# Kernel optimization log

Hardware: AMD Instinct MI355X
Metric: run time of the kernel (lower is better)

Reference implementation:

```python
import jax, jax.numpy as jnp
import numpy as np

B, R, S, T, D, DK = 256, 196, 200, 50, 512, 100


def setup_inputs() -> dict:
    key = jax.random.key(0)
    ks = jax.random.split(key, 20)
    inp = {
        'ifeature': jax.random.normal(ks[0], (B, R, D), jnp.float32),
        'tfeature_h': jax.random.normal(ks[1], (B, S, D), jnp.float32),
        'gfeature': jax.random.normal(ks[2], (B, S, D), jnp.float32),
        'efeature': jax.random.normal(ks[3], (B, T, D), jnp.float32),
    }
    # learned params (keras 'random_normal' init ~ stddev 0.05, 'zeros' for biases)
    lens = [R, S, S, T]
    for i in range(4):
        inp[f'w_vi{i}'] = 0.05 * jax.random.normal(ks[4 + 4 * i], (D, DK), jnp.float32)
        inp[f'w_vt{i}'] = 0.05 * jax.random.normal(ks[5 + 4 * i], (D, DK), jnp.float32)
        inp[f'w_p{i}'] = 0.05 * jax.random.normal(ks[6 + 4 * i], (2 * DK, 1), jnp.float32)
        inp[f'b{i}'] = jnp.zeros((lens[i],), jnp.float32)
    return inp


def _attend(feats, w_feat, vec, w_vec, w_p, b, vec_first):
    # feats: [B,N,D], vec: [B,D]. Score = concat(tanh parts) @ w_p + b.
    # concat+dense == split w_p into the two halves and add the partial scores.
    k = w_feat.shape[1]
    sf = jnp.tanh(jnp.einsum('bnd,dk->bnk', feats, w_feat))  # [B,N,k]
    sv = jnp.tanh(vec @ w_vec)                               # [B,k]
    if vec_first:
        wv, wf = w_p[:k, 0], w_p[k:, 0]
    else:
        wf, wv = w_p[:k, 0], w_p[k:, 0]
    score = sf @ wf + (sv @ wv)[:, None] + b                 # [B,N]
    p = jax.nn.softmax(score, axis=-1)
    return jnp.einsum('bn,bnd->bd', p, feats)                # [B,D]


def reference(ifeature, tfeature_h, gfeature, efeature,
              w_vi0, w_vt0, w_p0, b0,
              w_vi1, w_vt1, w_p1, b1,
              w_vi2, w_vt2, w_p2, b2,
              w_vi3, w_vt3, w_p3, b3):
    tfeature = jnp.mean(tfeature_h, axis=1)                  # [B,D]
    # block 0: attend over image regions, concat order (image, text)
    Vi = _attend(ifeature, w_vi0, tfeature, w_vt0, w_p0, b0, vec_first=False)
    # block 1: attend over text tokens, concat order (Vi, text)
    Vt = _attend(tfeature_h, w_vt1, Vi, w_vi1, w_p1, b1, vec_first=True)
    # block 2: attend over group feature with query Vi+Vt
    Vg = _attend(gfeature, w_vt2, Vi + Vt, w_vi2, w_p2, b2, vec_first=True)
    # block 3: attend over title feature with query Vi+Vt
    Ve = _attend(efeature, w_vt3, Vi + Vt, w_vi3, w_p3, b3, vec_first=True)
    return Vi + Vt + 0.5 * Vg + 0.5 * Ve
```

## Files before the change

### kernel.cpp

```cpp
#include <hip/hip_runtime.h>

#define DD 512
#define DKk 100
#define NT 7
#define CHUNK 16
#define MAXN 208
#define LDS_STRIDE 520

typedef __attribute__((ext_vector_type(8))) short short8;
typedef __attribute__((ext_vector_type(4))) short short4v;
typedef __attribute__((ext_vector_type(4))) float f32x4;

struct AttendArgs {
  const float* feats[4];
  const float* wfeat[4];
  const float* wf[4];
  const float* bias[4];
  int   N[4];
  float coef[4];
};

__device__ __forceinline__ short f2bf(float x) {
  unsigned u = __builtin_bit_cast(unsigned, x);
  unsigned r = (u + 0x7fffu + ((u >> 16) & 1u)) >> 16;
  return (short)r;
}

__device__ __forceinline__ float bf2f(unsigned short s) {
  unsigned u = ((unsigned)s) << 16;
  return __builtin_bit_cast(float, u);
}

__device__ __forceinline__ float fast_tanh(float x) {
  const float e = __expf(2.0f * x);
  return 1.0f - 2.0f / (e + 1.0f);
}

__global__ void wprep_kernel(AttendArgs args, unsigned short* __restrict__ wfrag) {
  const int a   = blockIdx.x >> 2;
  const int qtr = blockIdx.x & 3;
  const int tid = threadIdx.x;
  const int lane = tid & 63;
  const int m = lane & 15;
  const int q = lane >> 4;
  const int sub = tid >> 6;
  const int ks  = qtr * 4 + sub;
  __shared__ float wbuf[128 * DKk];
  const float* __restrict__ w = args.wfeat[a] + (size_t)qtr * 128 * DKk;
  #pragma unroll
  for (int i = 0; i < 50; ++i)
    wbuf[i * 256 + tid] = w[i * 256 + tid];
  __syncthreads();
  #pragma unroll
  for (int t = 0; t < NT; ++t) {
    const int col = t * 16 + m;
    short8 v;
    #pragma unroll
    for (int j = 0; j < 8; ++j) {
      const int drel = sub * 32 + q * 8 + j;
      v[j] = (col < DKk) ? f2bf(wbuf[drel * DKk + col]) : (short)0;
    }
    unsigned short* dst = wfrag + (size_t)(((a * NT + t) * 16 + ks) * 512) + lane * 8;
    *reinterpret_cast<short8*>(dst) = v;
  }
}

__global__ __launch_bounds__(512, 2)
void fused_kernel(AttendArgs args, const unsigned short* __restrict__ wfrag,
                  float* __restrict__ out) {
  const int a = blockIdx.x & 3;
  const int b = blockIdx.x >> 2;
  const int tid = threadIdx.x;
  const int lane = tid & 63;
  const int wave = tid >> 6;
  const int m = lane & 15;
  const int q = lane >> 4;
  const int N = args.N[a];
  const float* __restrict__ feats = args.feats[a] + (size_t)b * (size_t)N * DD;
  const float* __restrict__ wfp = args.wf[a];
  const float* __restrict__ bias = args.bias[a];

  __shared__ __align__(16) unsigned short f_lds[2][CHUNK][LDS_STRIDE];
  __shared__ float sc_part[8][MAXN];
  __shared__ __align__(16) float partial[8][DD];
  __shared__ float red[512];

  short8 bfrag[16];
  float wfv = 0.f;
  if (wave < NT) {
    const int col = wave * 16 + m;
    wfv = (col < DKk) ? wfp[col] : 0.f;
    const unsigned short* src = wfrag + (size_t)((a * NT + wave) * 16) * 512 + lane * 8;
    #pragma unroll
    for (int ks = 0; ks < 16; ++ks)
      bfrag[ks] = *reinterpret_cast<const short8*>(src + (size_t)ks * 512);
  } else {
    #pragma unroll
    for (int ks = 0; ks < 16; ++ks) bfrag[ks] = short8(0);
  }

  if (tid < MAXN) sc_part[7][tid] = (tid < N) ? bias[tid] : 0.f;
  {
    const f32x4 z = {0.f, 0.f, 0.f, 0.f};
    *reinterpret_cast<f32x4*>(&partial[wave][lane * 8])     = z;
    *reinterpret_cast<f32x4*>(&partial[wave][lane * 8 + 4]) = z;
  }

  const int nchunks = (N + CHUNK - 1) / CHUNK;

  auto accum = [&](int pb, int n0) {
    float* pp = &partial[wave][lane * 8];
    f32x4 lo = *reinterpret_cast<f32x4*>(pp);
    f32x4 hi = *reinterpret_cast<f32x4*>(pp + 4);
    {
      const int n1 = n0 + wave;
      const float s1 = sc_part[0][n1] + sc_part[1][n1] + sc_part[2][n1] + sc_part[3][n1]
                     + sc_part[4][n1] + sc_part[5][n1] + sc_part[6][n1] + sc_part[7][n1];
      const float e1 = __expf(s1);
      const short8 f1 = *reinterpret_cast<const short8*>(&f_lds[pb][wave][lane * 8]);
      #pragma unroll
      for (int j = 0; j < 4; ++j) {
        lo[j] = fmaf(e1, bf2f((unsigned short)f1[j]),     lo[j]);
        hi[j] = fmaf(e1, bf2f((unsigned short)f1[j + 4]), hi[j]);
      }
    }
    {
      const int n2 = n0 + wave + 8;
      const float s2 = sc_part[0][n2] + sc_part[1][n2] + sc_part[2][n2] + sc_part[3][n2]
                     + sc_part[4][n2] + sc_part[5][n2] + sc_part[6][n2] + sc_part[7][n2];
      const float e2 = __expf(s2);
      const short8 f2 = *reinterpret_cast<const short8*>(&f_lds[pb][wave + 8][lane * 8]);
      #pragma unroll
      for (int j = 0; j < 4; ++j) {
        lo[j] = fmaf(e2, bf2f((unsigned short)f2[j]),     lo[j]);
        hi[j] = fmaf(e2, bf2f((unsigned short)f2[j + 4]), hi[j]);
      }
    }
    *reinterpret_cast<f32x4*>(pp)     = lo;
    *reinterpret_cast<f32x4*>(pp + 4) = hi;
  };

  float4 pf[4];
  #pragma unroll
  for (int it = 0; it < 4; ++it) {
    const int idx = tid + it * 512;
    const int row = idx >> 7;
    const int c4 = idx & 127;
    pf[it] = (row < N)
      ? *reinterpret_cast<const float4*>(feats + (size_t)row * DD + (c4 << 2))
      : make_float4(0.f, 0.f, 0.f, 0.f);
  }

  for (int c = 0; c < nchunks; ++c) {
    const int bufc = c & 1;
    #pragma unroll
    for (int it = 0; it < 4; ++it) {
      const int idx = tid + it * 512;
      const int row = idx >> 7;
      const int c4 = idx & 127;
      short4v pk = { f2bf(pf[it].x), f2bf(pf[it].y), f2bf(pf[it].z), f2bf(pf[it].w) };
      *reinterpret_cast<short4v*>(&f_lds[bufc][row][c4 << 2]) = pk;
    }
    if (c + 1 < nchunks) {
      const int n0n = (c + 1) * CHUNK;
      #pragma unroll
      for (int it = 0; it < 4; ++it) {
        const int idx = tid + it * 512;
        const int row = n0n + (idx >> 7);
        const int c4 = idx & 127;
        pf[it] = (row < N)
          ? *reinterpret_cast<const float4*>(feats + (size_t)row * DD + (c4 << 2))
          : make_float4(0.f, 0.f, 0.f, 0.f);
      }
    }
    __syncthreads();

    if (wave < NT) {
      f32x4 acc = {0.f, 0.f, 0.f, 0.f};
      #pragma unroll
      for (int ks = 0; ks < 16; ++ks) {
        const short8 af = *reinterpret_cast<const short8*>(&f_lds[bufc][m][ks * 32 + q * 8]);
        acc = __builtin_amdgcn_mfma_f32_16x16x32_bf16(af, bfrag[ks], acc, 0, 0, 0);
      }
      float part[4];
      #pragma unroll
      for (int r = 0; r < 4; ++r) part[r] = fast_tanh(acc[r]) * wfv;
      #pragma unroll
      for (int mask = 1; mask <= 8; mask <<= 1) {
        #pragma unroll
        for (int r = 0; r < 4; ++r) part[r] += __shfl_xor(part[r], mask, 64);
      }
      if (m == 0) {
        #pragma unroll
        for (int r = 0; r < 4; ++r) sc_part[wave][c * 16 + q * 4 + r] = part[r];
      }
    }
    if (c > 0) accum(bufc ^ 1, (c - 1) * CHUNK);
    __syncthreads();
  }

  accum((nchunks - 1) & 1, (nchunks - 1) * CHUNK);
  __syncthreads();

  float e = 0.f;
  if (tid < N) {
    const float sval = sc_part[0][tid] + sc_part[1][tid] + sc_part[2][tid] + sc_part[3][tid]
                     + sc_part[4][tid] + sc_part[5][tid] + sc_part[6][tid] + sc_part[7][tid];
    e = __expf(sval);
  }
  red[tid] = e;
  __syncthreads();
  for (int s = 256; s > 0; s >>= 1) {
    if (tid < s) red[tid] += red[tid + s];
    __syncthreads();
  }
  const float scale = args.coef[a] / red[0];

  const float val = partial[0][tid] + partial[1][tid] + partial[2][tid] + partial[3][tid]
                  + partial[4][tid] + partial[5][tid] + partial[6][tid] + partial[7][tid];
  atomicAdd(&out[(size_t)b * DD + tid], val * scale);
}

extern "C" void kernel_launch(void* const* d_in, const int* in_sizes, int n_in,
                              void* d_out, int out_size, void* d_ws, size_t ws_size,
                              hipStream_t stream) {
  AttendArgs args;
  args.feats[0] = (const float*)d_in[0];
  args.wfeat[0] = (const float*)d_in[4];
  args.wf[0]    = (const float*)d_in[6];
  args.bias[0]  = (const float*)d_in[7];
  args.N[0] = 196; args.coef[0] = 1.0f;

  args.feats[1] = (const float*)d_in[1];
  args.wfeat[1] = (const float*)d_in[9];
  args.wf[1]    = (const float*)d_in[10] + 100;
  args.bias[1]  = (const float*)d_in[11];
  args.N[1] = 200; args.coef[1] = 1.0f;

  args.feats[2] = (const float*)d_in[2];
  args.wfeat[2] = (const float*)d_in[13];
  args.wf[2]    = (const float*)d_in[14] + 100;
  args.bias[2]  = (const float*)d_in[15];
  args.N[2] = 200; args.coef[2] = 0.5f;

  args.feats[3] = (const float*)d_in[3];
  args.wfeat[3] = (const float*)d_in[17];
  args.wf[3]    = (const float*)d_in[18] + 100;
  args.bias[3]  = (const float*)d_in[19];
  args.N[3] = 50;  args.coef[3] = 0.5f;

  unsigned short* wfrag = (unsigned short*)d_ws;

  hipMemsetAsync(d_out, 0, (size_t)out_size * sizeof(float), stream);
  wprep_kernel<<<dim3(16), dim3(256), 0, stream>>>(args, wfrag);
  fused_kernel<<<dim3(4 * 256), dim3(512), 0, stream>>>(args, wfrag, (float*)d_out);
}
```

Baseline: 366.7 us.

## Fold weight prep into fused kernel, DPP score reduction, leaner LDS softmax

Drops the separate weight-prep kernel: each block now loads and converts its MFMA weight fragments straight from global memory with strided scalar loads. It also swaps the shuffle-based score reduction for DPP adds, moves the softmax denominator into per-wave running sums instead of a tree reduction, lays partial scores out per row for vectorized reads, and changes the feature load mapping so each lane writes 8 contiguous bf16 values. Launch bounds are raised to 4 blocks per CU. These changes cut a kernel launch, synchronizations and LDS traffic, at the cost of redundant, uncoalesced weight reads in every block and possible register pressure from the higher occupancy target.

```diff
diff --git a/kernel.cpp b/kernel.cpp
--- a/kernel.cpp
+++ b/kernel.cpp
@@ -8,7 +8,6 @@
 #define LDS_STRIDE 520
 
 typedef __attribute__((ext_vector_type(8))) short short8;
-typedef __attribute__((ext_vector_type(4))) short short4v;
 typedef __attribute__((ext_vector_type(4))) float f32x4;
 
 struct AttendArgs {
@@ -25,49 +24,21 @@
   unsigned r = (u + 0x7fffu + ((u >> 16) & 1u)) >> 16;
   return (short)r;
 }
-
 __device__ __forceinline__ float bf2f(unsigned short s) {
   unsigned u = ((unsigned)s) << 16;
   return __builtin_bit_cast(float, u);
 }
-
 __device__ __forceinline__ float fast_tanh(float x) {
   const float e = __expf(2.0f * x);
   return 1.0f - 2.0f / (e + 1.0f);
 }
 
-__global__ void wprep_kernel(AttendArgs args, unsigned short* __restrict__ wfrag) {
-  const int a   = blockIdx.x >> 2;
-  const int qtr = blockIdx.x & 3;
-  const int tid = threadIdx.x;
-  const int lane = tid & 63;
-  const int m = lane & 15;
-  const int q = lane >> 4;
-  const int sub = tid >> 6;
-  const int ks  = qtr * 4 + sub;
-  __shared__ float wbuf[128 * DKk];
-  const float* __restrict__ w = args.wfeat[a] + (size_t)qtr * 128 * DKk;
-  #pragma unroll
-  for (int i = 0; i < 50; ++i)
-    wbuf[i * 256 + tid] = w[i * 256 + tid];
-  __syncthreads();
-  #pragma unroll
-  for (int t = 0; t < NT; ++t) {
-    const int col = t * 16 + m;
-    short8 v;
-    #pragma unroll
-    for (int j = 0; j < 8; ++j) {
-      const int drel = sub * 32 + q * 8 + j;
-      v[j] = (col < DKk) ? f2bf(wbuf[drel * DKk + col]) : (short)0;
-    }
-    unsigned short* dst = wfrag + (size_t)(((a * NT + t) * 16 + ks) * 512) + lane * 8;
-    *reinterpret_cast<short8*>(dst) = v;
-  }
-}
-
-__global__ __launch_bounds__(512, 2)
-void fused_kernel(AttendArgs args, const unsigned short* __restrict__ wfrag,
-                  float* __restrict__ out) {
+#define DPP_ADD(x, CTRL)                                                      \
+  (x) += __builtin_bit_cast(float, __builtin_amdgcn_update_dpp(               \
+             0, __builtin_bit_cast(int, (x)), (CTRL), 0xF, 0xF, true))
+
+__global__ __launch_bounds__(512, 4)
+void fused_kernel(AttendArgs args, float* __restrict__ out) {
   const int a = blockIdx.x & 3;
   const int b = blockIdx.x >> 2;
   const int tid = threadIdx.x;
@@ -77,100 +48,94 @@
   const int q = lane >> 4;
   const int N = args.N[a];
   const float* __restrict__ feats = args.feats[a] + (size_t)b * (size_t)N * DD;
-  const float* __restrict__ wfp = args.wf[a];
-  const float* __restrict__ bias = args.bias[a];
 
   __shared__ __align__(16) unsigned short f_lds[2][CHUNK][LDS_STRIDE];
-  __shared__ float sc_part[8][MAXN];
-  __shared__ __align__(16) float partial[8][DD];
-  __shared__ float red[512];
+  __shared__ __align__(16) float sc2[MAXN][8];
+  __shared__ __align__(16) float pA[8][256];
+  __shared__ __align__(16) float pB[8][256];
+  __shared__ float den8[8];
 
   short8 bfrag[16];
   float wfv = 0.f;
-  if (wave < NT) {
+  {
     const int col = wave * 16 + m;
-    wfv = (col < DKk) ? wfp[col] : 0.f;
-    const unsigned short* src = wfrag + (size_t)((a * NT + wave) * 16) * 512 + lane * 8;
+    const bool ok = (wave < NT) && (col < DKk);
+    if (ok) wfv = args.wf[a][col];
+    const float* __restrict__ wp = args.wfeat[a] + col;
     #pragma unroll
-    for (int ks = 0; ks < 16; ++ks)
-      bfrag[ks] = *reinterpret_cast<const short8*>(src + (size_t)ks * 512);
-  } else {
-    #pragma unroll
-    for (int ks = 0; ks < 16; ++ks) bfrag[ks] = short8(0);
-  }
-
-  if (tid < MAXN) sc_part[7][tid] = (tid < N) ? bias[tid] : 0.f;
+    for (int ks = 0; ks < 16; ++ks) {
+      short8 v;
+      #pragma unroll
+      for (int j = 0; j < 8; ++j)
+        v[j] = ok ? f2bf(wp[(size_t)(ks * 32 + q * 8 + j) * DKk]) : (short)0;
+      bfrag[ks] = v;
+    }
+  }
+
+  if (tid < MAXN) sc2[tid][7] = (tid < N) ? args.bias[a][tid] : -1e30f;
   {
     const f32x4 z = {0.f, 0.f, 0.f, 0.f};
-    *reinterpret_cast<f32x4*>(&partial[wave][lane * 8])     = z;
-    *reinterpret_cast<f32x4*>(&partial[wave][lane * 8 + 4]) = z;
+    *reinterpret_cast<f32x4*>(&pA[wave][lane * 4]) = z;
+    *reinterpret_cast<f32x4*>(&pB[wave][lane * 4]) = z;
   }
 
   const int nchunks = (N + CHUNK - 1) / CHUNK;
+  float den = 0.f;
 
   auto accum = [&](int pb, int n0) {
-    float* pp = &partial[wave][lane * 8];
-    f32x4 lo = *reinterpret_cast<f32x4*>(pp);
-    f32x4 hi = *reinterpret_cast<f32x4*>(pp + 4);
-    {
-      const int n1 = n0 + wave;
-      const float s1 = sc_part[0][n1] + sc_part[1][n1] + sc_part[2][n1] + sc_part[3][n1]
-                     + sc_part[4][n1] + sc_part[5][n1] + sc_part[6][n1] + sc_part[7][n1];
-      const float e1 = __expf(s1);
-      const short8 f1 = *reinterpret_cast<const short8*>(&f_lds[pb][wave][lane * 8]);
-      #pragma unroll
-      for (int j = 0; j < 4; ++j) {
-        lo[j] = fmaf(e1, bf2f((unsigned short)f1[j]),     lo[j]);
-        hi[j] = fmaf(e1, bf2f((unsigned short)f1[j + 4]), hi[j]);
-      }
-    }
-    {
-      const int n2 = n0 + wave + 8;
-      const float s2 = sc_part[0][n2] + sc_part[1][n2] + sc_part[2][n2] + sc_part[3][n2]
-                     + sc_part[4][n2] + sc_part[5][n2] + sc_part[6][n2] + sc_part[7][n2];
-      const float e2 = __expf(s2);
-      const short8 f2 = *reinterpret_cast<const short8*>(&f_lds[pb][wave + 8][lane * 8]);
-      #pragma unroll
-      for (int j = 0; j < 4; ++j) {
-        lo[j] = fmaf(e2, bf2f((unsigned short)f2[j]),     lo[j]);
-        hi[j] = fmaf(e2, bf2f((unsigned short)f2[j + 4]), hi[j]);
-      }
-    }
-    *reinterpret_cast<f32x4*>(pp)     = lo;
-    *reinterpret_cast<f32x4*>(pp + 4) = hi;
+    const int n1 = n0 + wave, n2 = n0 + wave + 8;
+    const f32x4 sa1 = *reinterpret_cast<const f32x4*>(&sc2[n1][0]);
+    const f32x4 sb1 = *reinterpret_cast<const f32x4*>(&sc2[n1][4]);
+    const f32x4 sa2 = *reinterpret_cast<const f32x4*>(&sc2[n2][0]);
+    const f32x4 sb2 = *reinterpret_cast<const f32x4*>(&sc2[n2][4]);
+    const float e1 = __expf(sa1[0] + sa1[1] + sa1[2] + sa1[3] +
+                            sb1[0] + sb1[1] + sb1[2] + sb1[3]);
+    const float e2 = __expf(sa2[0] + sa2[1] + sa2[2] + sa2[3] +
+                            sb2[0] + sb2[1] + sb2[2] + sb2[3]);
+    den += e1 + e2;
+    const short8 f1 = *reinterpret_cast<const short8*>(&f_lds[pb][wave][lane * 8]);
+    const short8 f2 = *reinterpret_cast<const short8*>(&f_lds[pb][wave + 8][lane * 8]);
+    f32x4 lo = *reinterpret_cast<const f32x4*>(&pA[wave][lane * 4]);
+    f32x4 hi = *reinterpret_cast<const f32x4*>(&pB[wave][lane * 4]);
+    #pragma unroll
+    for (int j = 0; j < 4; ++j) {
+      lo[j] = fmaf(e1, bf2f((unsigned short)f1[j]),
+              fmaf(e2, bf2f((unsigned short)f2[j]), lo[j]));
+      hi[j] = fmaf(e1, bf2f((unsigned short)f1[j + 4]),
+              fmaf(e2, bf2f((unsigned short)f2[j + 4]), hi[j]));
+    }
+    *reinterpret_cast<f32x4*>(&pA[wave][lane * 4]) = lo;
+    *reinterpret_cast<f32x4*>(&pB[wave][lane * 4]) = hi;
   };
 
   float4 pf[4];
   #pragma unroll
-  for (int it = 0; it < 4; ++it) {
-    const int idx = tid + it * 512;
-    const int row = idx >> 7;
-    const int c4 = idx & 127;
-    pf[it] = (row < N)
-      ? *reinterpret_cast<const float4*>(feats + (size_t)row * DD + (c4 << 2))
-      : make_float4(0.f, 0.f, 0.f, 0.f);
+  for (int h = 0; h < 2; ++h) {
+    const int row = wave + h * 8;
+    const float* src = feats + (size_t)row * DD + lane * 8;
+    const bool ok = row < N;
+    pf[2 * h]     = ok ? *reinterpret_cast<const float4*>(src)     : make_float4(0.f, 0.f, 0.f, 0.f);
+    pf[2 * h + 1] = ok ? *reinterpret_cast<const float4*>(src + 4) : make_float4(0.f, 0.f, 0.f, 0.f);
   }
 
   for (int c = 0; c < nchunks; ++c) {
     const int bufc = c & 1;
     #pragma unroll
-    for (int it = 0; it < 4; ++it) {
-      const int idx = tid + it * 512;
-      const int row = idx >> 7;
-      const int c4 = idx & 127;
-      short4v pk = { f2bf(pf[it].x), f2bf(pf[it].y), f2bf(pf[it].z), f2bf(pf[it].w) };
-      *reinterpret_cast<short4v*>(&f_lds[bufc][row][c4 << 2]) = pk;
+    for (int h = 0; h < 2; ++h) {
+      const float4 va = pf[2 * h], vb = pf[2 * h + 1];
+      short8 pk = { f2bf(va.x), f2bf(va.y), f2bf(va.z), f2bf(va.w),
+                    f2bf(vb.x), f2bf(vb.y), f2bf(vb.z), f2bf(vb.w) };
+      *reinterpret_cast<short8*>(&f_lds[bufc][wave + h * 8][lane * 8]) = pk;
     }
     if (c + 1 < nchunks) {
       const int n0n = (c + 1) * CHUNK;
       #pragma unroll
-      for (int it = 0; it < 4; ++it) {
-        const int idx = tid + it * 512;
-        const int row = n0n + (idx >> 7);
-        const int c4 = idx & 127;
-        pf[it] = (row < N)
-          ? *reinterpret_cast<const float4*>(feats + (size_t)row * DD + (c4 << 2))
-          : make_float4(0.f, 0.f, 0.f, 0.f);
+      for (int h = 0; h < 2; ++h) {
+        const int row = n0n + wave + h * 8;
+        const float* src = feats + (size_t)row * DD + lane * 8;
+        const bool ok = row < N;
+        pf[2 * h]     = ok ? *reinterpret_cast<const float4*>(src)     : make_float4(0.f, 0.f, 0.f, 0.f);
+        pf[2 * h + 1] = ok ? *reinterpret_cast<const float4*>(src + 4) : make_float4(0.f, 0.f, 0.f, 0.f);
       }
     }
     __syncthreads();
@@ -182,42 +147,37 @@
         const short8 af = *reinterpret_cast<const short8*>(&f_lds[bufc][m][ks * 32 + q * 8]);
         acc = __builtin_amdgcn_mfma_f32_16x16x32_bf16(af, bfrag[ks], acc, 0, 0, 0);
       }
-      float part[4];
-      #pragma unroll
-      for (int r = 0; r < 4; ++r) part[r] = fast_tanh(acc[r]) * wfv;
-      #pragma unroll
-      for (int mask = 1; mask <= 8; mask <<= 1) {
-        #pragma unroll
-        for (int r = 0; r < 4; ++r) part[r] += __shfl_xor(part[r], mask, 64);
-      }
-      if (m == 0) {
-        #pragma unroll
-        for (int r = 0; r < 4; ++r) sc_part[wave][c * 16 + q * 4 + r] = part[r];
-      }
+      float p0 = fast_tanh(acc[0]) * wfv;
+      float p1 = fast_tanh(acc[1]) * wfv;
+      float p2 = fast_tanh(acc[2]) * wfv;
+      float p3 = fast_tanh(acc[3]) * wfv;
+      DPP_ADD(p0, 0xB1);  DPP_ADD(p1, 0xB1);  DPP_ADD(p2, 0xB1);  DPP_ADD(p3, 0xB1);
+      DPP_ADD(p0, 0x4E);  DPP_ADD(p1, 0x4E);  DPP_ADD(p2, 0x4E);  DPP_ADD(p3, 0x4E);
+      DPP_ADD(p0, 0x141); DPP_ADD(p1, 0x141); DPP_ADD(p2, 0x141); DPP_ADD(p3, 0x141);
+      DPP_ADD(p0, 0x140); DPP_ADD(p1, 0x140); DPP_ADD(p2, 0x140); DPP_ADD(p3, 0x140);
+      float pv = p0;
+      pv = (m == 1) ? p1 : pv;
+      pv = (m == 2) ? p2 : pv;
+      pv = (m == 3) ? p3 : pv;
+      if (m < 4) sc2[c * 16 + q * 4 + m][wave] = pv;
     }
     if (c > 0) accum(bufc ^ 1, (c - 1) * CHUNK);
     __syncthreads();
   }
 
   accum((nchunks - 1) & 1, (nchunks - 1) * CHUNK);
+  if (lane == 0) den8[wave] = den;
   __syncthreads();
 
-  float e = 0.f;
-  if (tid < N) {
-    const float sval = sc_part[0][tid] + sc_part[1][tid] + sc_part[2][tid] + sc_part[3][tid]
-                     + sc_part[4][tid] + sc_part[5][tid] + sc_part[6][tid] + sc_part[7][tid];
-    e = __expf(sval);
-  }
-  red[tid] = e;
-  __syncthreads();
-  for (int s = 256; s > 0; s >>= 1) {
-    if (tid < s) red[tid] += red[tid + s];
-    __syncthreads();
-  }
-  const float scale = args.coef[a] / red[0];
-
-  const float val = partial[0][tid] + partial[1][tid] + partial[2][tid] + partial[3][tid]
-                  + partial[4][tid] + partial[5][tid] + partial[6][tid] + partial[7][tid];
+  const float denom = den8[0] + den8[1] + den8[2] + den8[3] +
+                      den8[4] + den8[5] + den8[6] + den8[7];
+  const float scale = args.coef[a] / denom;
+
+  const int g = tid >> 3, rr = tid & 7;
+  const float* cp = (rr < 4) ? &pA[0][g * 4 + rr] : &pB[0][g * 4 + (rr - 4)];
+  float val = 0.f;
+  #pragma unroll
+  for (int w = 0; w < 8; ++w) val += cp[w * 256];
   atomicAdd(&out[(size_t)b * DD + tid], val * scale);
 }
 
@@ -249,9 +209,6 @@
   args.bias[3]  = (const float*)d_in[19];
   args.N[3] = 50;  args.coef[3] = 0.5f;
 
-  unsigned short* wfrag = (unsigned short*)d_ws;
-
   hipMemsetAsync(d_out, 0, (size_t)out_size * sizeof(float), stream);
-  wprep_kernel<<<dim3(16), dim3(256), 0, stream>>>(args, wfrag);
-  fused_kernel<<<dim3(4 * 256), dim3(512), 0, stream>>>(args, wfrag, (float*)d_out);
-}
+  fused_kernel<<<dim3(4 * 256), dim3(512), 0, stream>>>(args, (float*)d_out);
+}
```

Measured after the change: 449.7 us. 22.6% more time.
